# Kernel optimization log

Measured on AMD Instinct MI355X. Metric: run time of the kernel, lower is better.

## Reference

```python
import jax, jax.numpy as jnp
import numpy as np

B, S, D_IN, D_OUT, H = 4, 2048, 768, 768, 12
DH = D_OUT // H


def setup_inputs() -> dict:
    key = jax.random.key(0)
    ks = jax.random.split(key, 6)
    x = jax.random.normal(ks[0], (B, S, D_IN), dtype=jnp.float32)
    # causal mask: True above the diagonal means "masked out" (filled with -inf)
    mask = jnp.triu(jnp.ones((S, S), dtype=bool), k=1)
    sc = 1.0 / np.sqrt(D_IN)
    Wq = jax.random.normal(ks[1], (D_IN, D_OUT), dtype=jnp.float32) * sc
    Wk = jax.random.normal(ks[2], (D_IN, D_OUT), dtype=jnp.float32) * sc
    Wv = jax.random.normal(ks[3], (D_IN, D_OUT), dtype=jnp.float32) * sc
    Wo = jax.random.normal(ks[4], (D_OUT, D_OUT), dtype=jnp.float32) * (1.0 / np.sqrt(D_OUT))
    bo = jnp.zeros((D_OUT,), dtype=jnp.float32)
    return {"input_tensor": x, "mask": mask, "Wq": Wq, "Wk": Wk, "Wv": Wv, "Wo": Wo, "bo": bo}


def reference(input_tensor, mask, Wq, Wk, Wv, Wo, bo):
    b, n, _ = input_tensor.shape
    # projections -> [b, h, n, dh]
    q = (input_tensor @ Wq).reshape(b, n, H, DH).transpose(0, 2, 1, 3)
    k = (input_tensor @ Wk).reshape(b, n, H, DH).transpose(0, 2, 1, 3)
    v = (input_tensor @ Wv).reshape(b, n, H, DH).transpose(0, 2, 1, 3)
    # scores [b, h, n, n]
    scores = jnp.einsum('bhqd,bhkd->bhqk', q, k)
    scores = jnp.where(mask[:n, :n], -jnp.inf, scores)
    attn = jax.nn.softmax(scores / np.sqrt(DH), axis=-1)
    ctx = jnp.einsum('bhqk,bhkd->bhqd', attn, v)
    ctx = ctx.transpose(0, 2, 1, 3).reshape(b, n, D_OUT)
    return ctx @ Wo + bo
```

## Files before the change

### kernel.cpp

```cpp
#include <hip/hip_runtime.h>
#include <hip/hip_bf16.h>
#include <math.h>

typedef __attribute__((ext_vector_type(4))) float f32x4;
typedef __attribute__((ext_vector_type(8))) short s16x8;
typedef __attribute__((ext_vector_type(8))) unsigned short u16x8;

#define B_ 4
#define S_ 2048
#define DIN 768
#define DOUT 768
#define H_ 12
#define DH_ 64
#define M_ (B_*S_)

__device__ __forceinline__ unsigned short f2bf(float f) {
  union { float f; unsigned u; } v; v.f = f;
  unsigned r = v.u + 0x7fffu + ((v.u >> 16) & 1u);
  return (unsigned short)(r >> 16);
}


__global__ __launch_bounds__(256) void cast_x(const float* __restrict__ X,
                                              unsigned short* __restrict__ Xb) {
  size_t i = ((size_t)blockIdx.x * 256 + threadIdx.x) * 8;
  float4 a = *(const float4*)&X[i];
  float4 b = *(const float4*)&X[i + 4];
  u16x8 v;
  v[0] = f2bf(a.x); v[1] = f2bf(a.y); v[2] = f2bf(a.z); v[3] = f2bf(a.w);
  v[4] = f2bf(b.x); v[5] = f2bf(b.y); v[6] = f2bf(b.z); v[7] = f2bf(b.w);
  *(u16x8*)&Xb[i] = v;
}

__global__ __launch_bounds__(256) void tcast_w(
    const float* __restrict__ W0, const float* __restrict__ W1,
    const float* __restrict__ W2, const float* __restrict__ W3,
    unsigned short* __restrict__ Wt) {
  __shared__ float t[32][33];
  const float* W = blockIdx.z == 0 ? W0 : blockIdx.z == 1 ? W1
                 : blockIdx.z == 2 ? W2 : W3;
  unsigned short* Out = Wt + (size_t)blockIdx.z * DOUT * DIN;
  const int n0 = blockIdx.x * 32, k0 = blockIdx.y * 32;
  const int tx = threadIdx.x & 31, ty = threadIdx.x >> 5;
#pragma unroll
  for (int i = 0; i < 32; i += 8)
    t[ty + i][tx] = W[(size_t)(k0 + ty + i) * DOUT + n0 + tx];
  __syncthreads();
#pragma unroll
  for (int i = 0; i < 32; i += 8)
    Out[(size_t)(n0 + ty + i) * DIN + k0 + tx] = f2bf(t[tx][ty + i]);
}


#define BKC 32

__device__ __forceinline__ void stage_tile(
    const unsigned short* __restrict__ g, int row0, int k0,
    unsigned short* lds, int tid)
{
#pragma unroll
  for (int it = 0; it < 2; ++it) {
    int s = it * 256 + tid;
    int row = s >> 2, sc = s & 3;
    int gc = sc ^ ((row >> 1) & 3);
    const unsigned short* gsrc = g + (size_t)(row0 + row) * 768 + k0 + gc * 8;
    unsigned short* dst = lds + (size_t)(it * 256 + (tid & ~63)) * 8;
    __builtin_amdgcn_global_load_lds(
        (const __attribute__((address_space(1))) void*)gsrc,
        (__attribute__((address_space(3))) void*)dst, 16, 0, 0);
  }
}

__device__ __forceinline__ void gemm_core(
    const unsigned short* __restrict__ A, const unsigned short* __restrict__ Bt,
    int m0, int n0, unsigned short* As, unsigned short* Bs,
    f32x4 acc[4][4], int tid)
{
  const int lane = tid & 63;
  const int col_l = lane & 15, quad = lane >> 4;
  const int w = tid >> 6;
  const int wm = (w & 1) * 64, wn = (w >> 1) * 64;
  for (int k0 = 0; k0 < 768; k0 += BKC) {
    __syncthreads();
    stage_tile(A, m0, k0, As, tid);
    stage_tile(Bt, n0, k0, Bs, tid);
    __syncthreads();
    s16x8 af[4], bf[4];
#pragma unroll
    for (int t = 0; t < 4; ++t) {
      int ar = wm + t * 16 + col_l;
      af[t] = *(const s16x8*)&As[ar * 32 + (quad ^ ((ar >> 1) & 3)) * 8];
      int br = wn + t * 16 + col_l;
      bf[t] = *(const s16x8*)&Bs[br * 32 + (quad ^ ((br >> 1) & 3)) * 8];
    }
#pragma unroll
    for (int mt = 0; mt < 4; ++mt)
#pragma unroll
      for (int nt = 0; nt < 4; ++nt)
        acc[mt][nt] = __builtin_amdgcn_mfma_f32_16x16x32_bf16(
            af[mt], bf[nt], acc[mt][nt], 0, 0, 0);
  }
}

__global__ __launch_bounds__(256) void proj_mfma(
    const unsigned short* __restrict__ Xb, const unsigned short* __restrict__ Wt,
    unsigned short* __restrict__ Qo, unsigned short* __restrict__ Ko,
    unsigned short* __restrict__ Vo)
{
  __shared__ unsigned short As[128 * 32];
  __shared__ unsigned short Bs[128 * 32];
  const int tid = threadIdx.x;
  const int m0 = blockIdx.y * 128, n0 = blockIdx.x * 128;
  const int z = blockIdx.z;
  const unsigned short* Bw = Wt + (size_t)z * DOUT * DIN;
  unsigned short* Out = z == 0 ? Qo : z == 1 ? Ko : Vo;
  const float scale = z == 0 ? 0.125f : 1.0f;

  f32x4 acc[4][4] = {};
  gemm_core(Xb, Bw, m0, n0, As, Bs, acc, tid);

  const int lane = tid & 63, w = tid >> 6;
  const int col_l = lane & 15, quad = lane >> 4;
  const int wm = (w & 1) * 64, wn = (w >> 1) * 64;
  if (z == 2) {
    const int mblk = m0 + wm;
    const int b = mblk >> 11, sblk = mblk & (S_ - 1);
#pragma unroll
    for (int mt = 0; mt < 4; ++mt) {
      const int slot = (mt >> 1) * 32 + quad * 8 + (mt & 1) * 4;
#pragma unroll
      for (int nt = 0; nt < 4; ++nt) {
        int n = n0 + wn + nt * 16 + col_l;
        int h = n >> 6, d = n & 63;
        ushort4 v;
        v.x = f2bf(acc[mt][nt][0]); v.y = f2bf(acc[mt][nt][1]);
        v.z = f2bf(acc[mt][nt][2]); v.w = f2bf(acc[mt][nt][3]);
        *(ushort4*)&Out[((size_t)(b * H_ + h) * DH_ + d) * S_ + sblk + slot] = v;
      }
    }
  } else {
#pragma unroll
    for (int mt = 0; mt < 4; ++mt)
#pragma unroll
      for (int nt = 0; nt < 4; ++nt) {
        int n = n0 + wn + nt * 16 + col_l;
        int h = n >> 6, d = n & 63;
#pragma unroll
        for (int r = 0; r < 4; ++r) {
          int m = m0 + wm + mt * 16 + quad * 4 + r;
          int b = m >> 11, s = m & (S_ - 1);
          Out[((size_t)(b * H_ + h) * S_ + s) * DH_ + d] = f2bf(acc[mt][nt][r] * scale);
        }
      }
  }
}

__global__ __launch_bounds__(256) void out_mfma(
    const unsigned short* __restrict__ Cb, const unsigned short* __restrict__ Wt,
    const float* __restrict__ bo, float* __restrict__ Out)
{
  __shared__ unsigned short As[128 * 32];
  __shared__ unsigned short Bs[128 * 32];
  const int tid = threadIdx.x;
  const int m0 = blockIdx.y * 128, n0 = blockIdx.x * 128;

  f32x4 acc[4][4] = {};
  gemm_core(Cb, Wt, m0, n0, As, Bs, acc, tid);

  const int lane = tid & 63, w = tid >> 6;
  const int col_l = lane & 15, quad = lane >> 4;
  const int wm = (w & 1) * 64, wn = (w >> 1) * 64;
#pragma unroll
  for (int mt = 0; mt < 4; ++mt)
#pragma unroll
    for (int nt = 0; nt < 4; ++nt) {
      int n = n0 + wn + nt * 16 + col_l;
      float bias = bo[n];
#pragma unroll
      for (int r = 0; r < 4; ++r) {
        int m = m0 + wm + mt * 16 + quad * 4 + r;
        Out[(size_t)m * DOUT + n] = acc[mt][nt][r] + bias;
      }
    }
}


#define KSTR 72

union PK { uint2 u2[2]; s16x8 v; };

#define MFMA_BF16 __builtin_amdgcn_mfma_f32_16x16x32_bf16

__device__ __forceinline__ void exppack(const f32x4 sc[4], PK& p0, PK& p1) {
#pragma unroll
  for (int nc = 0; nc < 4; ++nc) {
    float e0 = __expf(sc[nc][0] - 12.0f);
    float e1 = __expf(sc[nc][1] - 12.0f);
    float e2 = __expf(sc[nc][2] - 12.0f);
    float e3 = __expf(sc[nc][3] - 12.0f);
    union { __hip_bfloat162 v; unsigned u; } lo, hi;
    lo.v = __float22bfloat162_rn(make_float2(e0, e1));
    hi.v = __float22bfloat162_rn(make_float2(e2, e3));
    uint2 pw; pw.x = lo.u; pw.y = hi.u;
    if (nc < 2) p0.u2[nc] = pw; else p1.u2[nc - 2] = pw;
  }
}

__global__ __launch_bounds__(256, 3) void attn_mfma(
    const unsigned short* __restrict__ Q, const unsigned short* __restrict__ K,
    const unsigned short* __restrict__ Vt, unsigned short* __restrict__ CTX)
{
  __shared__ unsigned short Ks[2][64 * KSTR];
  __shared__ unsigned short Vs[2][64 * KSTR];

  const int tid = threadIdx.x;
  const int lane = tid & 63;
  const int w = tid >> 6;
  const int col_l = lane & 15;
  const int quad = lane >> 4;
  const int b = blockIdx.z, h = blockIdx.y;
  const int p = blockIdx.x;
  const int q0A = p << 6, q0B = (31 - p) << 6;
  const int ntiles = 32 - p;
  const size_t bh = (size_t)(b * H_ + h);
  const unsigned short* Qg = Q + bh * S_ * DH_;
  const unsigned short* Kg = K + bh * S_ * DH_;
  const unsigned short* Vg = Vt + bh * DH_ * S_;

  const int qwA = q0A + (w << 4), qwB = q0B + (w << 4);
  s16x8 aqA0 = *(const s16x8*)&Qg[(size_t)(qwA + col_l) * DH_ + quad * 8];
  s16x8 aqA1 = *(const s16x8*)&Qg[(size_t)(qwA + col_l) * DH_ + 32 + quad * 8];
  s16x8 aqB0 = *(const s16x8*)&Qg[(size_t)(qwB + col_l) * DH_ + quad * 8];
  s16x8 aqB1 = *(const s16x8*)&Qg[(size_t)(qwB + col_l) * DH_ + 32 + quad * 8];

  const int krow = lane;
  const int vrow = tid >> 3;
  const int vslot = tid & 7;

  s16x8 kp0 = *(const s16x8*)&Kg[(size_t)krow * DH_ + w * 8];
  s16x8 kp1 = *(const s16x8*)&Kg[(size_t)krow * DH_ + (w + 4) * 8];
  s16x8 vp0 = *(const s16x8*)&Vg[(size_t)vrow * S_ + vslot * 8];
  s16x8 vp1 = *(const s16x8*)&Vg[(size_t)(vrow + 32) * S_ + vslot * 8];

  f32x4 oA[4] = {}, oB[4] = {}, lA = {}, lB = {};
  s16x8 bones;
#pragma unroll
  for (int i = 0; i < 8; ++i) bones[i] = (short)0x3F80;

  const int qrel = (w << 4) + col_l;

  for (int t = 0; t < ntiles; ++t) {
    unsigned short* KsB = &Ks[t & 1][0];
    unsigned short* VsB = &Vs[t & 1][0];
    *(s16x8*)&KsB[krow * KSTR + w * 8] = kp0;
    *(s16x8*)&KsB[krow * KSTR + (w + 4) * 8] = kp1;
    *(s16x8*)&VsB[vrow * KSTR + vslot * 8] = vp0;
    *(s16x8*)&VsB[(vrow + 32) * KSTR + vslot * 8] = vp1;
    __syncthreads();
    {
      const int jn = (t + 1 < ntiles ? t + 1 : t) << 6;
      kp0 = *(const s16x8*)&Kg[(size_t)(jn + krow) * DH_ + w * 8];
      kp1 = *(const s16x8*)&Kg[(size_t)(jn + krow) * DH_ + (w + 4) * 8];
      vp0 = *(const s16x8*)&Vg[(size_t)vrow * S_ + jn + vslot * 8];
      vp1 = *(const s16x8*)&Vg[(size_t)(vrow + 32) * S_ + jn + vslot * 8];
    }
    const bool doA = (t <= p);

    f32x4 scA[4], scB[4];
#pragma unroll
    for (int nc = 0; nc < 4; ++nc) {
      s16x8 k0 = *(const s16x8*)&KsB[(nc * 16 + col_l) * KSTR + quad * 8];
      s16x8 k1 = *(const s16x8*)&KsB[(nc * 16 + col_l) * KSTR + 32 + quad * 8];
      f32x4 a = {};
      a = MFMA_BF16(k0, aqB0, a, 0, 0, 0);
      a = MFMA_BF16(k1, aqB1, a, 0, 0, 0);
      scB[nc] = a;
      if (doA) {
        f32x4 c = {};
        c = MFMA_BF16(k0, aqA0, c, 0, 0, 0);
        c = MFMA_BF16(k1, aqA1, c, 0, 0, 0);
        scA[nc] = c;
      }
    }
    if (t == p) {
#pragma unroll
      for (int nc = 0; nc < 4; ++nc)
#pragma unroll
        for (int r = 0; r < 4; ++r)
          if (nc * 16 + quad * 4 + r > qrel) scA[nc][r] = -INFINITY;
    }
    if (t == ntiles - 1) {
#pragma unroll
      for (int nc = 0; nc < 4; ++nc)
#pragma unroll
        for (int r = 0; r < 4; ++r)
          if (nc * 16 + quad * 4 + r > qrel) scB[nc][r] = -INFINITY;
    }

    PK pA0, pA1, pB0, pB1;
    if (doA) exppack(scA, pA0, pA1);
    exppack(scB, pB0, pB1);

#pragma unroll
    for (int dc = 0; dc < 4; ++dc) {
      s16x8 b0 = *(const s16x8*)&VsB[(dc * 16 + col_l) * KSTR + quad * 8];
      s16x8 b1 = *(const s16x8*)&VsB[(dc * 16 + col_l) * KSTR + 32 + quad * 8];
      oB[dc] = MFMA_BF16(pB0.v, b0, oB[dc], 0, 0, 0);
      oB[dc] = MFMA_BF16(pB1.v, b1, oB[dc], 0, 0, 0);
      if (doA) {
        oA[dc] = MFMA_BF16(pA0.v, b0, oA[dc], 0, 0, 0);
        oA[dc] = MFMA_BF16(pA1.v, b1, oA[dc], 0, 0, 0);
      }
    }
    lB = MFMA_BF16(pB0.v, bones, lB, 0, 0, 0);
    lB = MFMA_BF16(pB1.v, bones, lB, 0, 0, 0);
    if (doA) {
      lA = MFMA_BF16(pA0.v, bones, lA, 0, 0, 0);
      lA = MFMA_BF16(pA1.v, bones, lA, 0, 0, 0);
    }
  }

  float liA[4], liB[4];
#pragma unroll
  for (int r = 0; r < 4; ++r) {
    liA[r] = 1.0f / lA[r];
    liB[r] = 1.0f / lB[r];
  }
#pragma unroll
  for (int dc = 0; dc < 4; ++dc)
#pragma unroll
    for (int r = 0; r < 4; ++r) {
      CTX[((size_t)(b * S_ + qwA + quad * 4 + r)) * DOUT + h * DH_ + dc * 16 + col_l]
          = f2bf(oA[dc][r] * liA[r]);
      CTX[((size_t)(b * S_ + qwB + quad * 4 + r)) * DOUT + h * DH_ + dc * 16 + col_l]
          = f2bf(oB[dc][r] * liB[r]);
    }
}


extern "C" void kernel_launch(void* const* d_in, const int* in_sizes, int n_in,
                              void* d_out, int out_size, void* d_ws, size_t ws_size,
                              hipStream_t stream) {
  const float* X  = (const float*)d_in[0];
  const float* Wq = (const float*)d_in[2];
  const float* Wk = (const float*)d_in[3];
  const float* Wv = (const float*)d_in[4];
  const float* Wo = (const float*)d_in[5];
  const float* bo = (const float*)d_in[6];
  float* out = (float*)d_out;

  unsigned short* Xb = (unsigned short*)d_ws;
  unsigned short* Wt = Xb + (size_t)M_ * DIN;
  unsigned short* Qb = Wt + (size_t)4 * DOUT * DIN;
  unsigned short* Kb = Qb + (size_t)M_ * DOUT;
  unsigned short* Vb = Kb + (size_t)M_ * DOUT;
  unsigned short* Cb = Vb + (size_t)M_ * DOUT;

  cast_x<<<dim3((M_ * DIN) / (256 * 8)), 256, 0, stream>>>(X, Xb);
  tcast_w<<<dim3(DOUT / 32, DIN / 32, 4), 256, 0, stream>>>(Wq, Wk, Wv, Wo, Wt);
  proj_mfma<<<dim3(DOUT / 128, M_ / 128, 3), 256, 0, stream>>>(Xb, Wt, Qb, Kb, Vb);
  attn_mfma<<<dim3(16, H_, B_), 256, 0, stream>>>(Qb, Kb, Vb, Cb);
  out_mfma<<<dim3(DOUT / 128, M_ / 128), 256, 0, stream>>>(
      Cb, Wt + (size_t)3 * DOUT * DIN, bo, out);
}
```

Measured before the change: 220.7 us.

## Double-buffer GEMM LDS staging, remap blocks for XCD locality, merge prep kernels

The GEMM main loop now double-buffers the A/B tiles in LDS. It prefetches the next k-slice with global_load_lds while computing the current one, using explicit vmcnt waits and barriers to hide global load latency. Block indices in proj, out and attn kernels are remapped so that consecutive blocks on the same XCD (id mod 8) share operand tiles, which should improve L2 reuse. The two cast/transpose kernels are merged into one launch to remove a launch gap. Costs are double the LDS per GEMM block and reliance on a hand-counted vmcnt value being correct.

```diff
diff --git a/kernel.cpp b/kernel.cpp
--- a/kernel.cpp
+++ b/kernel.cpp
@@ -21,38 +21,43 @@
 }
 
 
-__global__ __launch_bounds__(256) void cast_x(const float* __restrict__ X,
-                                              unsigned short* __restrict__ Xb) {
-  size_t i = ((size_t)blockIdx.x * 256 + threadIdx.x) * 8;
-  float4 a = *(const float4*)&X[i];
-  float4 b = *(const float4*)&X[i + 4];
-  u16x8 v;
-  v[0] = f2bf(a.x); v[1] = f2bf(a.y); v[2] = f2bf(a.z); v[3] = f2bf(a.w);
-  v[4] = f2bf(b.x); v[5] = f2bf(b.y); v[6] = f2bf(b.z); v[7] = f2bf(b.w);
-  *(u16x8*)&Xb[i] = v;
-}
-
-__global__ __launch_bounds__(256) void tcast_w(
+__global__ __launch_bounds__(256) void prep(
+    const float* __restrict__ X, unsigned short* __restrict__ Xb,
     const float* __restrict__ W0, const float* __restrict__ W1,
     const float* __restrict__ W2, const float* __restrict__ W3,
-    unsigned short* __restrict__ Wt) {
+    unsigned short* __restrict__ Wt)
+{
   __shared__ float t[32][33];
-  const float* W = blockIdx.z == 0 ? W0 : blockIdx.z == 1 ? W1
-                 : blockIdx.z == 2 ? W2 : W3;
-  unsigned short* Out = Wt + (size_t)blockIdx.z * DOUT * DIN;
-  const int n0 = blockIdx.x * 32, k0 = blockIdx.y * 32;
-  const int tx = threadIdx.x & 31, ty = threadIdx.x >> 5;
-#pragma unroll
-  for (int i = 0; i < 32; i += 8)
-    t[ty + i][tx] = W[(size_t)(k0 + ty + i) * DOUT + n0 + tx];
-  __syncthreads();
-#pragma unroll
-  for (int i = 0; i < 32; i += 8)
-    Out[(size_t)(n0 + ty + i) * DIN + k0 + tx] = f2bf(t[tx][ty + i]);
+  const int bid = blockIdx.x;
+  if (bid < 3072) {
+    size_t i = ((size_t)bid * 256 + threadIdx.x) * 8;
+    float4 a = *(const float4*)&X[i];
+    float4 b = *(const float4*)&X[i + 4];
+    u16x8 v;
+    v[0] = f2bf(a.x); v[1] = f2bf(a.y); v[2] = f2bf(a.z); v[3] = f2bf(a.w);
+    v[4] = f2bf(b.x); v[5] = f2bf(b.y); v[6] = f2bf(b.z); v[7] = f2bf(b.w);
+    *(u16x8*)&Xb[i] = v;
+  } else {
+    const int t4 = bid - 3072;
+    const int z = t4 / 576, rem = t4 - z * 576;
+    const int ky = rem / 24, nx = rem - ky * 24;
+    const float* W = z == 0 ? W0 : z == 1 ? W1 : z == 2 ? W2 : W3;
+    unsigned short* Out = Wt + (size_t)z * DOUT * DIN;
+    const int n0 = nx * 32, k0 = ky * 32;
+    const int tx = threadIdx.x & 31, ty = threadIdx.x >> 5;
+#pragma unroll
+    for (int i = 0; i < 32; i += 8)
+      t[ty + i][tx] = W[(size_t)(k0 + ty + i) * DOUT + n0 + tx];
+    __syncthreads();
+#pragma unroll
+    for (int i = 0; i < 32; i += 8)
+      Out[(size_t)(n0 + ty + i) * DIN + k0 + tx] = f2bf(t[tx][ty + i]);
+  }
 }
 
 
 #define BKC 32
+#define TILE_E (128 * BKC)
 
 __device__ __forceinline__ void stage_tile(
     const unsigned short* __restrict__ g, int row0, int k0,
@@ -80,18 +85,31 @@
   const int col_l = lane & 15, quad = lane >> 4;
   const int w = tid >> 6;
   const int wm = (w & 1) * 64, wn = (w >> 1) * 64;
+
+  stage_tile(A, m0, 0, As, tid);
+  stage_tile(Bt, n0, 0, Bs, tid);
+
+#pragma unroll 2
   for (int k0 = 0; k0 < 768; k0 += BKC) {
-    __syncthreads();
-    stage_tile(A, m0, k0, As, tid);
-    stage_tile(Bt, n0, k0, Bs, tid);
-    __syncthreads();
+    const int cur = (k0 / BKC) & 1;
+    const unsigned short* Asb = As + cur * TILE_E;
+    const unsigned short* Bsb = Bs + cur * TILE_E;
+    if (k0 + BKC < 768) {
+      stage_tile(A, m0, k0 + BKC, As + (cur ^ 1) * TILE_E, tid);
+      stage_tile(Bt, n0, k0 + BKC, Bs + (cur ^ 1) * TILE_E, tid);
+      asm volatile("s_waitcnt vmcnt(4)" ::: "memory");
+    } else {
+      asm volatile("s_waitcnt vmcnt(0)" ::: "memory");
+    }
+    __builtin_amdgcn_s_barrier();
+
     s16x8 af[4], bf[4];
 #pragma unroll
     for (int t = 0; t < 4; ++t) {
       int ar = wm + t * 16 + col_l;
-      af[t] = *(const s16x8*)&As[ar * 32 + (quad ^ ((ar >> 1) & 3)) * 8];
+      af[t] = *(const s16x8*)&Asb[ar * BKC + (quad ^ ((ar >> 1) & 3)) * 8];
       int br = wn + t * 16 + col_l;
-      bf[t] = *(const s16x8*)&Bs[br * 32 + (quad ^ ((br >> 1) & 3)) * 8];
+      bf[t] = *(const s16x8*)&Bsb[br * BKC + (quad ^ ((br >> 1) & 3)) * 8];
     }
 #pragma unroll
     for (int mt = 0; mt < 4; ++mt)
@@ -99,6 +117,8 @@
       for (int nt = 0; nt < 4; ++nt)
         acc[mt][nt] = __builtin_amdgcn_mfma_f32_16x16x32_bf16(
             af[mt], bf[nt], acc[mt][nt], 0, 0, 0);
+
+    __builtin_amdgcn_s_barrier();
   }
 }
 
@@ -107,11 +127,17 @@
     unsigned short* __restrict__ Qo, unsigned short* __restrict__ Ko,
     unsigned short* __restrict__ Vo)
 {
-  __shared__ unsigned short As[128 * 32];
-  __shared__ unsigned short Bs[128 * 32];
+  __shared__ unsigned short As[2 * TILE_E];
+  __shared__ unsigned short Bs[2 * TILE_E];
   const int tid = threadIdx.x;
-  const int m0 = blockIdx.y * 128, n0 = blockIdx.x * 128;
-  const int z = blockIdx.z;
+
+  const int orig = (blockIdx.z * 64 + blockIdx.y) * 6 + blockIdx.x;
+  const int id = (orig & 7) * 144 + (orig >> 3);
+  const int z = id / 384;
+  const int r = id - z * 384;
+  const int my = r / 6, nx = r - my * 6;
+  const int m0 = my * 128, n0 = nx * 128;
+
   const unsigned short* Bw = Wt + (size_t)z * DOUT * DIN;
   unsigned short* Out = z == 0 ? Qo : z == 1 ? Ko : Vo;
   const float scale = z == 0 ? 0.125f : 1.0f;
@@ -146,10 +172,10 @@
         int n = n0 + wn + nt * 16 + col_l;
         int h = n >> 6, d = n & 63;
 #pragma unroll
-        for (int r = 0; r < 4; ++r) {
-          int m = m0 + wm + mt * 16 + quad * 4 + r;
+        for (int r2 = 0; r2 < 4; ++r2) {
+          int m = m0 + wm + mt * 16 + quad * 4 + r2;
           int b = m >> 11, s = m & (S_ - 1);
-          Out[((size_t)(b * H_ + h) * S_ + s) * DH_ + d] = f2bf(acc[mt][nt][r] * scale);
+          Out[((size_t)(b * H_ + h) * S_ + s) * DH_ + d] = f2bf(acc[mt][nt][r2] * scale);
         }
       }
   }
@@ -159,10 +185,14 @@
     const unsigned short* __restrict__ Cb, const unsigned short* __restrict__ Wt,
     const float* __restrict__ bo, float* __restrict__ Out)
 {
-  __shared__ unsigned short As[128 * 32];
-  __shared__ unsigned short Bs[128 * 32];
+  __shared__ unsigned short As[2 * TILE_E];
+  __shared__ unsigned short Bs[2 * TILE_E];
   const int tid = threadIdx.x;
-  const int m0 = blockIdx.y * 128, n0 = blockIdx.x * 128;
+
+  const int orig = blockIdx.y * 6 + blockIdx.x;
+  const int id = (orig & 7) * 48 + (orig >> 3);
+  const int my = id / 6, nx = id - my * 6;
+  const int m0 = my * 128, n0 = nx * 128;
 
   f32x4 acc[4][4] = {};
   gemm_core(Cb, Wt, m0, n0, As, Bs, acc, tid);
@@ -218,14 +248,19 @@
   const int w = tid >> 6;
   const int col_l = lane & 15;
   const int quad = lane >> 4;
-  const int b = blockIdx.z, h = blockIdx.y;
-  const int p = blockIdx.x;
+
+  const int orig = (blockIdx.z * 12 + blockIdx.y) * 16 + blockIdx.x;
+  const int id = (orig & 7) * 96 + (orig >> 3);
+  const int p = id & 15;
+  const int bh = id >> 4;
+  const int h = bh % 12, b = bh / 12;
+
   const int q0A = p << 6, q0B = (31 - p) << 6;
   const int ntiles = 32 - p;
-  const size_t bh = (size_t)(b * H_ + h);
-  const unsigned short* Qg = Q + bh * S_ * DH_;
-  const unsigned short* Kg = K + bh * S_ * DH_;
-  const unsigned short* Vg = Vt + bh * DH_ * S_;
+  const size_t bhs = (size_t)(b * H_ + h);
+  const unsigned short* Qg = Q + bhs * S_ * DH_;
+  const unsigned short* Kg = K + bhs * S_ * DH_;
+  const unsigned short* Vg = Vt + bhs * DH_ * S_;
 
   const int qwA = q0A + (w << 4), qwB = q0B + (w << 4);
   s16x8 aqA0 = *(const s16x8*)&Qg[(size_t)(qwA + col_l) * DH_ + quad * 8];
@@ -356,8 +391,7 @@
   unsigned short* Vb = Kb + (size_t)M_ * DOUT;
   unsigned short* Cb = Vb + (size_t)M_ * DOUT;
 
-  cast_x<<<dim3((M_ * DIN) / (256 * 8)), 256, 0, stream>>>(X, Xb);
-  tcast_w<<<dim3(DOUT / 32, DIN / 32, 4), 256, 0, stream>>>(Wq, Wk, Wv, Wo, Wt);
+  prep<<<dim3(3072 + 2304), 256, 0, stream>>>(X, Xb, Wq, Wk, Wv, Wo, Wt);
   proj_mfma<<<dim3(DOUT / 128, M_ / 128, 3), 256, 0, stream>>>(Xb, Wt, Qb, Kb, Vb);
   attn_mfma<<<dim3(16, H_, B_), 256, 0, stream>>>(Qb, Kb, Vb, Cb);
   out_mfma<<<dim3(DOUT / 128, M_ / 128), 256, 0, stream>>>(
```

Result: no change. 218.3 us (-1.1%).
